# Performance work log

Hardware: AMD Instinct MI355X
Metric: run time of the kernel (lower is better)

The kernel has to match this reference:

```python
import jax, jax.numpy as jnp
import numpy as np

B, N, C = 4, 4096, 1024
H, M = 16, 64          # num_heads, num_landmarks
DH = C // H
SCALE = H ** (-0.5)    # faithful to source: num_heads**-0.5
LN_EPS = 1e-5


def setup_inputs() -> dict:
    key = jax.random.key(0)
    ks = jax.random.split(key, 8)
    s = 0.02
    return {
        "x": jax.random.normal(ks[0], (B, N, C), jnp.float32),
        "ln_w": jnp.ones((C,), jnp.float32),
        "ln_b": jnp.zeros((C,), jnp.float32),
        "qkv_w": jax.random.normal(ks[1], (3 * C, C), jnp.float32) * s,
        "qkv_b": jax.random.normal(ks[2], (3 * C,), jnp.float32) * s,
        "gamma_w": jax.random.normal(ks[3], (C, C), jnp.float32) * s,
        "gamma_b": jax.random.normal(ks[4], (C,), jnp.float32) * s,
        "proj_w": jax.random.normal(ks[5], (C, C), jnp.float32) * s,
        "proj_b": jax.random.normal(ks[6], (C,), jnp.float32) * s,
    }


def _iterative_inv(K, n_iter=6):
    # Newton-Schulz pseudo-inverse on [..., M, M]
    Id = jnp.eye(K.shape[-1], dtype=K.dtype)
    KA = jnp.abs(K)
    V0 = KA.sum(axis=-2, keepdims=True).max(axis=-1, keepdims=True)
    VI = KA.sum(axis=-1, keepdims=True).max(axis=-2, keepdims=True)
    V = jnp.swapaxes(K, -2, -1) / (V0 * VI)
    for _ in range(n_iter):
        KV = K @ V
        V = 0.25 * V @ (13.0 * Id - KV @ (15.0 * Id - KV @ (7.0 * Id - KV)))
    return V


def reference(x, ln_w, ln_b, qkv_w, qkv_b, gamma_w, gamma_b, proj_w, proj_b):
    # LayerNorm
    mu = x.mean(axis=-1, keepdims=True)
    var = x.var(axis=-1, keepdims=True)
    xn = (x - mu) * jax.lax.rsqrt(var + LN_EPS) * ln_w + ln_b
    # qkv: (B,N,3C) -> (3,B,H,N,DH)
    qkv = (xn @ qkv_w.T + qkv_b).reshape(B, N, 3, H, DH).transpose(2, 0, 3, 1, 4)
    q, k, v = qkv[0], qkv[1], qkv[2]
    # landmarks: mean-pool segments of length N//M, then scale
    q_lm = q.reshape(B, H, M, N // M, DH).mean(axis=-2) * SCALE  # (B,H,M,DH)
    k_lm = k.reshape(B, H, M, N // M, DH).mean(axis=-2) * SCALE
    attn1 = jax.nn.softmax(jnp.einsum('bhnd,bhmd->bhnm', q, k_lm), axis=-1)    # (B,H,N,M)
    attn2 = jax.nn.softmax(jnp.einsum('bhmd,bhld->bhml', q_lm, k_lm), axis=-1)  # (B,H,M,M)
    attn3 = jax.nn.softmax(jnp.einsum('bhmd,bhnd->bhmn', q_lm, k), axis=-1)    # (B,H,M,N)
    attn2_inv = _iterative_inv(attn2)
    out = attn1 @ (attn2_inv @ (attn3 @ v))            # (B,H,N,DH)
    out = out.transpose(0, 2, 1, 3).reshape(B, N, C)
    out = out @ gamma_w.T + gamma_b                    # LipNorm=True branch
    out = out @ proj_w.T + proj_b                      # proj (dropout p=0 is identity)
    return out
```

## Files before the change

### kernel.cpp

```cpp
#include <hip/hip_runtime.h>
#include <stdint.h>

typedef unsigned short u16;
typedef short bf16x8 __attribute__((ext_vector_type(8)));
typedef float f32x4 __attribute__((ext_vector_type(4)));

#define MFMA16(a, b, c) __builtin_amdgcn_mfma_f32_16x16x32_bf16((a), (b), (c), 0, 0, 0)

static __device__ __forceinline__ float bfu2f(u16 u) {
  union { unsigned int i; float f; } z; z.i = ((unsigned int)u) << 16; return z.f;
}
static __device__ __forceinline__ u16 f2bfu(float f) {
  union { float f; unsigned int i; } z; z.f = f;
  unsigned int i = z.i;
  return (u16)((i + 0x7fffu + ((i >> 16) & 1u)) >> 16);
}

__device__ __forceinline__ void gload_lds16(const void* g, void* l) {
  __builtin_amdgcn_global_load_lds((const __attribute__((address_space(1))) void*)g,
                                   (__attribute__((address_space(3))) void*)l, 16, 0, 0);
}

__global__ __launch_bounds__(256) void prep_kernel(
    const float* __restrict__ x, const float* __restrict__ lw,
    const float* __restrict__ lb, u16* __restrict__ xn,
    const float* __restrict__ qkvw, u16* __restrict__ QKVW,
    const float* __restrict__ projw, u16* __restrict__ PW,
    const float* __restrict__ G, u16* __restrict__ GT,
    const float* __restrict__ gb, const float* __restrict__ pb,
    float* __restrict__ b2) {
  int blk = blockIdx.x;
  int t = threadIdx.x;
  if (blk < 16384) {
    int row = blk;
    const float4* xr = (const float4*)(x + (size_t)row * 1024);
    float4 v = xr[t];
    float s = v.x + v.y + v.z + v.w;
    float ss = v.x * v.x + v.y * v.y + v.z * v.z + v.w * v.w;
#pragma unroll
    for (int m = 1; m < 64; m <<= 1) { s += __shfl_xor(s, m); ss += __shfl_xor(ss, m); }
    __shared__ float sb[4], ssb[4];
    int lane = t & 63, wvi = t >> 6;
    if (lane == 0) { sb[wvi] = s; ssb[wvi] = ss; }
    __syncthreads();
    s = sb[0] + sb[1] + sb[2] + sb[3];
    ss = ssb[0] + ssb[1] + ssb[2] + ssb[3];
    float mu = s * (1.0f / 1024.0f);
    float var = ss * (1.0f / 1024.0f) - mu * mu;
    float rstd = rsqrtf(var + 1e-5f);
    float4 wv4 = ((const float4*)lw)[t];
    float4 bv4 = ((const float4*)lb)[t];
    ushort4 o;
    o.x = f2bfu((v.x - mu) * rstd * wv4.x + bv4.x);
    o.y = f2bfu((v.y - mu) * rstd * wv4.y + bv4.y);
    o.z = f2bfu((v.z - mu) * rstd * wv4.z + bv4.z);
    o.w = f2bfu((v.w - mu) * rstd * wv4.w + bv4.w);
    ((ushort4*)xn)[(size_t)row * 256 + t] = o;
  } else if (blk < 18432) {
    int idx = (blk - 16384) * 256 + t;
    for (int i = idx; i < 1048576; i += 524288) {
      int j = i << 2;
      const float* s2; u16* d; int off;
      if (j < 3145728) { s2 = qkvw; d = QKVW; off = j; }
      else             { s2 = projw; d = PW; off = j - 3145728; }
      float4 v = *(const float4*)(s2 + off);
      ushort4 o;
      o.x = f2bfu(v.x); o.y = f2bfu(v.y); o.z = f2bfu(v.z); o.w = f2bfu(v.w);
      *(ushort4*)(d + off) = o;
    }
  } else if (blk < 18688) {
    __shared__ float tt[64][65];
    int tg = blk - 18432;
    int tr = (tg >> 4) * 64, tc = (tg & 15) * 64;
    int l = t & 63, y = t >> 6;
    for (int r = y; r < 64; r += 4)
      tt[r][l] = G[(size_t)(tr + r) * 1024 + tc + l];
    __syncthreads();
    for (int rr = y; rr < 64; rr += 4)
      GT[(size_t)(tc + rr) * 1024 + tr + l] = f2bfu(tt[l][rr]);
  } else {
    int i = (blk - 18688) * 256 + t;
    const float4* pr = (const float4*)(projw + (size_t)i * 1024);
    const float4* g4 = (const float4*)gb;
    float s = 0.f;
    for (int k = 0; k < 256; ++k) {
      float4 a = pr[k], b = g4[k];
      s += a.x * b.x + a.y * b.y + a.z * b.z + a.w * b.w;
    }
    b2[i] = s + pb[i];
  }
}

template <int MODE>
__global__ __launch_bounds__(512, 2) void gemm_bt(
    const u16* __restrict__ A, const u16* __restrict__ Bw,
    const float* __restrict__ bias,
    float* __restrict__ Cf, u16* __restrict__ Cb,
    u16* __restrict__ Qo, u16* __restrict__ Ko, u16* __restrict__ Vo,
    float* __restrict__ qlmf, u16* __restrict__ qlmb,
    float* __restrict__ klmf, u16* __restrict__ klmb,
    int M, int N, int K) {
  __shared__ __attribute__((aligned(16))) u16 As[2][16384];
  __shared__ __attribute__((aligned(16))) u16 Bs[2][16384];
  int tid = threadIdx.x;
  int lane = tid & 63;
  int w = tid >> 6;
  int wr = w >> 2, wc = w & 3;
  int r16 = lane & 15, hi = lane >> 4;
  int l8 = lane >> 3, li = lane & 7;

  int nwg = gridDim.x * gridDim.y;
  int flat = blockIdx.y * gridDim.x + blockIdx.x;
  int q8 = nwg >> 3;
  int swz = (flat & 7) * q8 + (flat >> 3);
  int bx = swz % gridDim.x, by = swz / gridDim.x;

  const char* Abase = (const char*)(A + (size_t)by * 256 * K);
  const char* Bbase = (const char*)(Bw + (size_t)bx * 256 * K);
  size_t rowbytes = (size_t)K * 2;
  int colsw = (li ^ l8) << 4;
  int nkt = K >> 6;

  f32x4 z4 = {0.f, 0.f, 0.f, 0.f};
  f32x4 acc[8][4];
#pragma unroll
  for (int m = 0; m < 8; ++m)
#pragma unroll
    for (int n = 0; n < 4; ++n) acc[m][n] = z4;

#define SG_A(buf, t, r0)                                                      \
  gload_lds16(Abase + (size_t)((r0) + w * 8 + l8) * rowbytes + ((t) << 7) +   \
                  colsw,                                                      \
              (char*)As[buf] + ((r0) + w * 8) * 128)
#define SG_B(buf, t, r0)                                                      \
  gload_lds16(Bbase + (size_t)((r0) + w * 8 + l8) * rowbytes + ((t) << 7) +   \
                  colsw,                                                      \
              (char*)Bs[buf] + ((r0) + w * 8) * 128)

  SG_A(0, 0, 0); SG_A(0, 0, 64); SG_A(0, 0, 128); SG_A(0, 0, 192);
  SG_B(0, 0, 0); SG_B(0, 0, 64); SG_B(0, 0, 128); SG_B(0, 0, 192);
  SG_A(1, 1, 0); SG_A(1, 1, 128); SG_B(1, 1, 0); SG_B(1, 1, 64);
  SG_A(1, 1, 64); SG_A(1, 1, 192);
  asm volatile("s_waitcnt vmcnt(6)" ::: "memory");
  __builtin_amdgcn_s_barrier();
  __builtin_amdgcn_sched_barrier(0);

  int buf = 0;
  bf16x8 af[4][2], bfr[4][2];

#define LDA(mh)                                                               \
  _Pragma("unroll") for (int m = 0; m < 4; ++m) {                             \
    int row = wr * 128 + (mh) * 64 + m * 16 + r16;                            \
    int sw = (row & 7) << 4;                                                  \
    _Pragma("unroll") for (int kk = 0; kk < 2; ++kk)                          \
        af[m][kk] = *(const bf16x8*)(ab + row * 128 +                         \
                                     (((kk << 6) | (hi << 4)) ^ sw));         \
  }
#define LDB(nh)                                                               \
  _Pragma("unroll") for (int n = 0; n < 2; ++n) {                             \
    int row = wc * 64 + (nh) * 32 + n * 16 + r16;                             \
    int sw = (row & 7) << 4;                                                  \
    _Pragma("unroll") for (int kk = 0; kk < 2; ++kk)                          \
        bfr[(nh) * 2 + n][kk] = *(const bf16x8*)(ab2 + row * 128 +            \
                                     (((kk << 6) | (hi << 4)) ^ sw));         \
  }
#define MM(mh, nh)                                                            \
  __builtin_amdgcn_s_setprio(1);                                              \
  _Pragma("unroll") for (int kk = 0; kk < 2; ++kk)                            \
      _Pragma("unroll") for (int m = 0; m < 4; ++m)                           \
          _Pragma("unroll") for (int n = 0; n < 2; ++n)                       \
              acc[(mh) * 4 + m][(nh) * 2 + n] =                               \
      MFMA16(af[m][kk], bfr[(nh) * 2 + n][kk], acc[(mh) * 4 + m][(nh) * 2 + n]); \
  __builtin_amdgcn_s_setprio(0)

#define BAR1                                                                  \
  __builtin_amdgcn_s_barrier();                                               \
  __builtin_amdgcn_sched_barrier(0)
#define BAR2                                                                  \
  __builtin_amdgcn_sched_barrier(0);                                          \
  __builtin_amdgcn_s_barrier();                                               \
  __builtin_amdgcn_sched_barrier(0)

  for (int t = 0; t < nkt; ++t) {
    const char* ab = (const char*)As[buf];
    const char* ab2 = (const char*)Bs[buf];
    bool s1 = (t + 1 < nkt), s2 = (t + 2 < nkt);
    LDA(0);
    LDB(0);
    if (s1) { SG_B(buf ^ 1, t + 1, 128); SG_B(buf ^ 1, t + 1, 192); }
    BAR1;
    MM(0, 0);
    BAR2;
    LDB(1);
    if (s2) { SG_A(buf, t + 2, 0); SG_A(buf, t + 2, 128); }
    BAR1;
    MM(0, 1);
    BAR2;
    LDA(1);
    if (s2) { SG_B(buf, t + 2, 0); SG_B(buf, t + 2, 64); }
    BAR1;
    MM(1, 0);
    BAR2;
    if (s2) { SG_A(buf, t + 2, 64); SG_A(buf, t + 2, 192); }
    BAR1;
    MM(1, 1);
    __builtin_amdgcn_sched_barrier(0);
    if (s2) {
      asm volatile("s_waitcnt vmcnt(6)" ::: "memory");
    } else {
      asm volatile("s_waitcnt vmcnt(0)" ::: "memory");
    }
    __builtin_amdgcn_s_barrier();
    __builtin_amdgcn_sched_barrier(0);
    buf ^= 1;
  }
#undef SG_A
#undef SG_B
#undef LDA
#undef LDB
#undef MM
#undef BAR1
#undef BAR2

#pragma unroll
  for (int m = 0; m < 8; ++m)
#pragma unroll
    for (int n = 0; n < 4; ++n) {
      int row0 = by * 256 + wr * 128 + m * 16 + hi * 4;
      int col = bx * 256 + wc * 64 + n * 16 + r16;
      if (MODE == 2) {
        int jt = col >> 10;
        int h = (col >> 6) & 15, dh = col & 63;
        int bb = row0 >> 12, nt0 = row0 & 4095;
        float bcol = bias[col];
        if (jt == 2) {
          ushort4 o;
          o.x = f2bfu(acc[m][n][0] + bcol);
          o.y = f2bfu(acc[m][n][1] + bcol);
          o.z = f2bfu(acc[m][n][2] + bcol);
          o.w = f2bfu(acc[m][n][3] + bcol);
          *(ushort4*)&Vo[(((size_t)bb * 16 + h) * 64 + dh) * 4096 + nt0] = o;
        } else {
          u16* dst = (jt == 0) ? Qo : Ko;
#pragma unroll
          for (int r = 0; r < 4; ++r)
            dst[(((size_t)bb * 16 + h) * 4096 + nt0 + r) * 64 + dh] =
                f2bfu(acc[m][n][r] + bcol);
        }
      } else {
        float bcol = bias[col];
#pragma unroll
        for (int r = 0; r < 4; ++r) {
          int row = row0 + r;
          Cf[(size_t)row * N + col] = acc[m][n][r] + bcol;
        }
      }
    }

  if (MODE == 2) {
    int jt = bx >> 2;
    if (jt < 2) {
      float* fo = (jt == 0) ? qlmf : klmf;
      u16* bo = (jt == 0) ? qlmb : klmb;
      int bb = by >> 4;
      int segb = (by * 4) & 63;
#pragma unroll
      for (int mh = 0; mh < 2; ++mh) {
        int seg = segb + wr * 2 + mh;
#pragma unroll
        for (int n = 0; n < 4; ++n) {
          int col = bx * 256 + wc * 64 + n * 16 + r16;
          float s = 0.f;
#pragma unroll
          for (int m = 0; m < 4; ++m)
#pragma unroll
            for (int r = 0; r < 4; ++r) s += acc[mh * 4 + m][n][r];
          s += 16.0f * bias[col];
          s += __shfl_xor(s, 16);
          s += __shfl_xor(s, 32);
          if (hi == 0) {
            int h = (col >> 6) & 15, dh = col & 63;
            float val = s * (0.25f / 64.0f);
            size_t o = (((size_t)bb * 16 + h) * 64 + seg) * 64 + dh;
            fo[o] = val;
            bo[o] = f2bfu(val);
          }
        }
      }
    }
  }
}

__global__ __launch_bounds__(256) void attn3_pv_kernel(
    const u16* __restrict__ qlmb, const u16* __restrict__ Kmat,
    const u16* __restrict__ Vt, float* __restrict__ Upart,
    float* __restrict__ rspart,
    const u16* __restrict__ Aw2, const u16* __restrict__ Bw2,
    float* __restrict__ Cp) {
  __shared__ __attribute__((aligned(16))) u16 Elds[4][8192];
  int tid = threadIdx.x, lane = tid & 63, w = tid >> 6;
  int r16 = lane & 15, hi = lane >> 4;
  int l8 = lane >> 3, li = lane & 7;

  if (blockIdx.x >= 4) {
    int wid = (blockIdx.x - 4) * 64 + blockIdx.y;
    u16* As = &Elds[0][0];
    u16* Bs = &Elds[1][0];
    int wr = w >> 1, wc = w & 1;
    int kz = wid >> 6, bxw = wid & 7, byw = (wid >> 3) & 7;
    const char* Abase = (const char*)(Aw2 + (size_t)byw * 131072 + kz * 256);
    const char* Bbase = (const char*)(Bw2 + (size_t)bxw * 131072 + kz * 256);
    int colsw = (li ^ l8) << 4;
    f32x4 z4 = {0.f, 0.f, 0.f, 0.f};
    f32x4 acc[4][4];
#pragma unroll
    for (int m = 0; m < 4; ++m)
#pragma unroll
      for (int n = 0; n < 4; ++n) acc[m][n] = z4;
    for (int kt = 0; kt < 4; ++kt) {
      int kb = kt << 7;
#pragma unroll
      for (int i = 0; i < 4; ++i) {
        int c = w * 4 + i;
        int rr = c * 8 + l8;
        gload_lds16(Abase + (size_t)rr * 2048 + kb + colsw, (char*)As + c * 1024);
        gload_lds16(Bbase + (size_t)rr * 2048 + kb + colsw, (char*)Bs + c * 1024);
      }
      __syncthreads();
      int sw = (lane & 7) << 4;
#pragma unroll
      for (int kk = 0; kk < 2; ++kk) {
        int kby = (kk << 6) + (hi << 4);
        bf16x8 af[4], bfr[4];
#pragma unroll
        for (int m = 0; m < 4; ++m) {
          int row = wr * 64 + m * 16 + r16;
          af[m] = *(const bf16x8*)((const char*)As + row * 128 + (kby ^ sw));
        }
#pragma unroll
        for (int n = 0; n < 4; ++n) {
          int row = wc * 64 + n * 16 + r16;
          bfr[n] = *(const bf16x8*)((const char*)Bs + row * 128 + (kby ^ sw));
        }
#pragma unroll
        for (int m = 0; m < 4; ++m)
#pragma unroll
          for (int n = 0; n < 4; ++n) acc[m][n] = MFMA16(af[m], bfr[n], acc[m][n]);
      }
      __syncthreads();
    }
#pragma unroll
    for (int m = 0; m < 4; ++m)
#pragma unroll
      for (int n = 0; n < 4; ++n)
#pragma unroll
        for (int r = 0; r < 4; ++r) {
          int row = byw * 128 + wr * 64 + m * 16 + hi * 4 + r;
          int col = bxw * 128 + wc * 64 + n * 16 + r16;
          Cp[(size_t)kz * 1048576 + (size_t)row * 1024 + col] = acc[m][n][r];
        }
    return;
  }

  int chunk = blockIdx.x, bh = blockIdx.y;
  const u16* vtb = Vt + (size_t)bh * 262144;
  const u16* qb = qlmb + (size_t)bh * 4096;
  u16* eb = &Elds[w][0];
  f32x4 z4 = {0.f, 0.f, 0.f, 0.f};

  bf16x8 afr[4][2];
#pragma unroll
  for (int m = 0; m < 4; ++m)
#pragma unroll
    for (int kk = 0; kk < 2; ++kk)
      afr[m][kk] = *(const bf16x8*)(qb + (m * 16 + r16) * 64 + kk * 32 + hi * 8);

  float rs[4][4] = {};
  f32x4 U[4][4];
#pragma unroll
  for (int m = 0; m < 4; ++m)
#pragma unroll
    for (int df = 0; df < 4; ++df) U[m][df] = z4;

  for (int bat = 0; bat < 2; ++bat) {
    int keybase = chunk * 1024 + bat * 512 + w * 128;
    const u16* kb = Kmat + ((size_t)bh * 4096 + keybase) * 64;
    for (int cf = 0; cf < 8; ++cf) {
      f32x4 S[4] = {z4, z4, z4, z4};
#pragma unroll
      for (int kk = 0; kk < 2; ++kk) {
        bf16x8 bfr = *(const bf16x8*)(kb + (size_t)(cf * 16 + r16) * 64 + kk * 32 + hi * 8);
#pragma unroll
        for (int m = 0; m < 4; ++m) S[m] = MFMA16(afr[m][kk], bfr, S[m]);
      }
#pragma unroll
      for (int m = 0; m < 4; ++m)
#pragma unroll
        for (int r = 0; r < 4; ++r) {
          float e = __expf(S[m][r]);
          rs[m][r] += e;
          int row = m * 16 + hi * 4 + r;
          int key = cf * 16 + r16;
          *(u16*)((char*)eb + row * 256 + ((key * 2) ^ ((row & 7) << 4))) = f2bfu(e);
        }
    }
    __syncthreads();
    for (int ks = 0; ks < 4; ++ks) {
      bf16x8 ea[4];
#pragma unroll
      for (int m = 0; m < 4; ++m) {
        int row = m * 16 + r16;
        ea[m] = *(const bf16x8*)((char*)eb + row * 256 + (((ks * 32 + hi * 8) * 2) ^ ((row & 7) << 4)));
      }
#pragma unroll
      for (int df = 0; df < 4; ++df) {
        bf16x8 vb8 = *(const bf16x8*)(vtb + (size_t)(df * 16 + r16) * 4096 +
                                      keybase + ks * 32 + hi * 8);
#pragma unroll
        for (int m = 0; m < 4; ++m) U[m][df] = MFMA16(ea[m], vb8, U[m][df]);
      }
    }
    __syncthreads();
  }

#pragma unroll
  for (int m = 0; m < 4; ++m)
#pragma unroll
    for (int r = 0; r < 4; ++r) {
      float v = rs[m][r];
      v += __shfl_xor(v, 1); v += __shfl_xor(v, 2);
      v += __shfl_xor(v, 4); v += __shfl_xor(v, 8);
      rs[m][r] = v;
    }
  if (r16 == 0) {
    float* rp = rspart + (((size_t)bh * 4 + chunk) * 4 + w) * 64;
#pragma unroll
    for (int m = 0; m < 4; ++m)
#pragma unroll
      for (int r = 0; r < 4; ++r) rp[m * 16 + hi * 4 + r] = rs[m][r];
  }
  float* up = Upart + (((size_t)bh * 4 + chunk) * 4 + w) * 4096;
#pragma unroll
  for (int m = 0; m < 4; ++m)
#pragma unroll
    for (int df = 0; df < 4; ++df)
#pragma unroll
      for (int r = 0; r < 4; ++r)
        up[(m * 16 + hi * 4 + r) * 64 + df * 16 + r16] = U[m][df][r];
}

__device__ __forceinline__ void mm64d(const float (*AT)[68], const float (*Bm)[68],
                                      float (*C)[68], float (*CT)[68],
                                      float alpha, float dconst, bool dmode,
                                      int tid) {
  int tr = (tid >> 4) << 1;
  int tc = (tid & 15) << 2;
  float acc[2][4] = {};
#pragma unroll 4
  for (int k = 0; k < 64; ++k) {
    float2 av = *(const float2*)&AT[k][tr];
    float4 bv = *(const float4*)&Bm[k][tc];
    float aa[2] = {av.x, av.y};
    float bb[4] = {bv.x, bv.y, bv.z, bv.w};
#pragma unroll
    for (int i = 0; i < 2; ++i)
#pragma unroll
      for (int j = 0; j < 4; ++j) acc[i][j] = fmaf(aa[i], bb[j], acc[i][j]);
  }
#pragma unroll
  for (int i = 0; i < 2; ++i)
#pragma unroll
    for (int j = 0; j < 4; ++j) {
      float vv = acc[i][j] * alpha;
      if (CT) CT[tc + j][tr + i] = vv;
      C[tr + i][tc + j] =
          dmode ? (((tr + i) == (tc + j)) ? dconst - vv : -vv) : vv;
    }
}

__global__ __launch_bounds__(512) void combine_ns_kernel(
    const float* __restrict__ Upart, const float* __restrict__ rspart,
    const float* __restrict__ qlmf, const float* __restrict__ klmf,
    u16* __restrict__ WT, const float* __restrict__ Cp,
    u16* __restrict__ W2b) {
  int tid = threadIdx.x;
  if (blockIdx.x >= 64) {
    int idx4 = (blockIdx.x - 64) * 512 + tid;
    const float4* p = (const float4*)Cp + idx4;
    float4 s = p[0];
    float4 b = p[262144], c = p[524288], d = p[786432];
    s.x += b.x + c.x + d.x;
    s.y += b.y + c.y + d.y;
    s.z += b.z + c.z + d.z;
    s.w += b.w + c.w + d.w;
    ushort4 o;
    o.x = f2bfu(s.x); o.y = f2bfu(s.y); o.z = f2bfu(s.z); o.w = f2bfu(s.w);
    ((ushort4*)W2b)[idx4] = o;
    return;
  }
  __shared__ __attribute__((aligned(16))) float A2T[64][68];
  __shared__ __attribute__((aligned(16))) float Vv[64][68];
  __shared__ __attribute__((aligned(16))) float VT[64][68];
  __shared__ __attribute__((aligned(16))) float KV[64][68];
  __shared__ __attribute__((aligned(16))) float KVT[64][68];
  __shared__ __attribute__((aligned(16))) float T2[64][68];
  __shared__ __attribute__((aligned(16))) float T4[64][68];
  __shared__ __attribute__((aligned(16))) float Tm[64][68];
  __shared__ float rsum[64], redbuf[64];
  __shared__ float scal;
  int bh = blockIdx.x;

  if (tid < 64) {
    float s = 0.f;
    const float* rp = rspart + (size_t)bh * 1024 + tid;
#pragma unroll 8
    for (int p = 0; p < 16; ++p) s += rp[p * 64];
    rsum[tid] = s;
  }
  __syncthreads();
  for (int idx4 = tid; idx4 < 1024; idx4 += 512) {
    const float4* up = (const float4*)(Upart + (size_t)bh * 65536) + idx4;
    float4 s = {0.f, 0.f, 0.f, 0.f};
#pragma unroll 8
    for (int p = 0; p < 16; ++p) {
      float4 v = up[p * 1024];
      s.x += v.x; s.y += v.y; s.z += v.z; s.w += v.w;
    }
    float inv = 1.0f / rsum[idx4 >> 4];
    int r = idx4 >> 4, c0 = (idx4 & 15) << 2;
    Tm[r][c0] = s.x * inv; Tm[r][c0 + 1] = s.y * inv;
    Tm[r][c0 + 2] = s.z * inv; Tm[r][c0 + 3] = s.w * inv;
  }
  for (int idx = tid; idx < 4096; idx += 512) {
    int r = idx >> 6, c = idx & 63;
    Vv[c][r] = qlmf[(size_t)bh * 4096 + idx];
    VT[c][r] = klmf[(size_t)bh * 4096 + idx];
  }
  __syncthreads();
  mm64d(&Vv[0], &VT[0], &T2[0], nullptr, 1.0f, 0.f, false, tid);
  __syncthreads();
  {
    int row = tid >> 3, sub = tid & 7, cb = sub * 8;
    float mx = -1e30f;
#pragma unroll
    for (int j = 0; j < 8; ++j) mx = fmaxf(mx, T2[row][cb + j]);
    mx = fmaxf(mx, __shfl_xor(mx, 1));
    mx = fmaxf(mx, __shfl_xor(mx, 2));
    mx = fmaxf(mx, __shfl_xor(mx, 4));
    float e[8];
    float s = 0.f;
#pragma unroll
    for (int j = 0; j < 8; ++j) { e[j] = __expf(T2[row][cb + j] - mx); s += e[j]; }
    s += __shfl_xor(s, 1); s += __shfl_xor(s, 2); s += __shfl_xor(s, 4);
    float inv = 1.f / s;
#pragma unroll
    for (int j = 0; j < 8; ++j) {
      float p = e[j] * inv;
      T2[row][cb + j] = p;
      A2T[cb + j][row] = p;
    }
  }
  __syncthreads();
  {
    int col = tid >> 3, sub = tid & 7;
    float cs = 0.f;
#pragma unroll
    for (int j = 0; j < 8; ++j) cs += T2[sub * 8 + j][col];
    cs += __shfl_xor(cs, 1); cs += __shfl_xor(cs, 2); cs += __shfl_xor(cs, 4);
    if (sub == 0) redbuf[col] = cs;
  }
  __syncthreads();
  if (tid < 64) {
    float v0 = redbuf[tid];
#pragma unroll
    for (int m = 1; m < 64; m <<= 1) v0 = fmaxf(v0, __shfl_xor(v0, m));
    if (tid == 0) scal = 1.0f / v0;
  }
  __syncthreads();
  for (int idx = tid; idx < 4096; idx += 512) {
    int r = idx >> 6, c = idx & 63;
    Vv[r][c] = A2T[r][c] * scal;
    VT[r][c] = T2[r][c] * scal;
  }
  __syncthreads();
  float (*Vt_r)[68] = VT;
  float (*Vt_w)[68] = KV;
#pragma unroll 1
  for (int it = 0; it < 6; ++it) {
    mm64d(&A2T[0], &Vv[0], &T2[0], &KVT[0], 1.0f, 7.0f, true, tid);
    __syncthreads();
    mm64d(&KVT[0], &T2[0], &T4[0], nullptr, 1.0f, 15.0f, true, tid);
    __syncthreads();
    mm64d(&KVT[0], &T4[0], &T2[0], nullptr, 1.0f, 13.0f, true, tid);
    __syncthreads();
    mm64d(Vt_r, &T2[0], &Vv[0], Vt_w, 0.25f, 0.f, false, tid);
    __syncthreads();
    float (*tmp)[68] = Vt_r; Vt_r = Vt_w; Vt_w = tmp;
  }
  mm64d(Vt_r, &Tm[0], &T2[0], nullptr, 1.0f, 0.f, false, tid);
  __syncthreads();
  for (int idx = tid; idx < 4096; idx += 512) {
    int r = idx >> 6, c = idx & 63;
    WT[(size_t)bh * 4096 + c * 64 + r] = f2bfu(T2[r][c]);
  }
}

__global__ __launch_bounds__(256) void attn1_out_kernel(
    const u16* __restrict__ Q, const u16* __restrict__ klmb,
    const u16* __restrict__ WT, u16* __restrict__ AO) {
  __shared__ __attribute__((aligned(16))) u16 Elds[4][2048];
  int bh = blockIdx.y;
  int b = bh >> 4, h = bh & 15;
  int tid = threadIdx.x, lane = tid & 63, w = tid >> 6;
  int r16 = lane & 15, hi = lane >> 4;
  int rowbase = blockIdx.x * 128 + w * 32;
  const u16* qb = Q + ((size_t)bh * 4096 + rowbase) * 64;
  const u16* kb = klmb + (size_t)bh * 4096;
  const u16* wtb = WT + (size_t)bh * 4096;
  u16* eb = &Elds[w][0];
  f32x4 z4 = {0.f, 0.f, 0.f, 0.f};

  bf16x8 afr[2][2];
#pragma unroll
  for (int mi = 0; mi < 2; ++mi)
#pragma unroll
    for (int kk = 0; kk < 2; ++kk)
      afr[mi][kk] = *(const bf16x8*)(qb + (mi * 16 + r16) * 64 + kk * 32 + hi * 8);

  float rs[2][4] = {};
  for (int cf = 0; cf < 4; ++cf) {
    f32x4 S[2] = {z4, z4};
#pragma unroll
    for (int kk = 0; kk < 2; ++kk) {
      bf16x8 bfr = *(const bf16x8*)(kb + (cf * 16 + r16) * 64 + kk * 32 + hi * 8);
#pragma unroll
      for (int mi = 0; mi < 2; ++mi) S[mi] = MFMA16(afr[mi][kk], bfr, S[mi]);
    }
#pragma unroll
    for (int mi = 0; mi < 2; ++mi)
#pragma unroll
      for (int r = 0; r < 4; ++r) {
        float e = __expf(S[mi][r]);
        rs[mi][r] += e;
        int row = mi * 16 + hi * 4 + r;
        int key = cf * 16 + r16;
        *(u16*)((char*)eb + row * 128 + ((key * 2) ^ ((row & 7) << 4))) = f2bfu(e);
      }
  }
#pragma unroll
  for (int mi = 0; mi < 2; ++mi)
#pragma unroll
    for (int r = 0; r < 4; ++r) {
      float v = rs[mi][r];
      v += __shfl_xor(v, 1); v += __shfl_xor(v, 2);
      v += __shfl_xor(v, 4); v += __shfl_xor(v, 8);
      rs[mi][r] = v;
    }
  __syncthreads();

  f32x4 O[2][4];
#pragma unroll
  for (int mi = 0; mi < 2; ++mi)
#pragma unroll
    for (int df = 0; df < 4; ++df) O[mi][df] = z4;
  for (int ks = 0; ks < 2; ++ks) {
    bf16x8 ea[2];
#pragma unroll
    for (int mi = 0; mi < 2; ++mi) {
      int row = mi * 16 + r16;
      ea[mi] = *(const bf16x8*)((char*)eb + row * 128 + (((ks * 32 + hi * 8) * 2) ^ ((row & 7) << 4)));
    }
#pragma unroll
    for (int df = 0; df < 4; ++df) {
      bf16x8 wfr = *(const bf16x8*)(wtb + (df * 16 + r16) * 64 + ks * 32 + hi * 8);
#pragma unroll
      for (int mi = 0; mi < 2; ++mi) O[mi][df] = MFMA16(ea[mi], wfr, O[mi][df]);
    }
  }
#pragma unroll
  for (int mi = 0; mi < 2; ++mi)
#pragma unroll
    for (int df = 0; df < 4; ++df)
#pragma unroll
      for (int r = 0; r < 4; ++r) {
        int row = mi * 16 + hi * 4 + r;
        int n = rowbase + row;
        int col = h * 64 + df * 16 + r16;
        float val = O[mi][df][r] / rs[mi][r];
        AO[((size_t)b * 4096 + n) * 1024 + col] = f2bfu(val);
      }
}

extern "C" void kernel_launch(void* const* d_in, const int* in_sizes, int n_in,
                              void* d_out, int out_size, void* d_ws, size_t ws_size,
                              hipStream_t stream) {
  (void)in_sizes; (void)n_in; (void)out_size; (void)ws_size;
  const float* x       = (const float*)d_in[0];
  const float* ln_w    = (const float*)d_in[1];
  const float* ln_b    = (const float*)d_in[2];
  const float* qkv_w   = (const float*)d_in[3];
  const float* qkv_b   = (const float*)d_in[4];
  const float* gamma_w = (const float*)d_in[5];
  const float* gamma_b = (const float*)d_in[6];
  const float* proj_w  = (const float*)d_in[7];
  const float* proj_b  = (const float*)d_in[8];

  char* ws = (char*)d_ws;
  u16* XN     = (u16*)(ws + 0);
  u16* Qb     = (u16*)(ws + 33554432);
  u16* Kb     = (u16*)(ws + 67108864);
  u16* Vb     = (u16*)(ws + 100663296);
  u16* QKVW   = (u16*)(ws + 134217728);
  u16* GTb    = (u16*)(ws + 140509184);
  u16* PW     = (u16*)(ws + 142606336);
  float* QLMF = (float*)(ws + 144703488);
  float* KLMF = (float*)(ws + 145752064);
  u16* QLMB   = (u16*)(ws + 146800640);
  u16* KLMB   = (u16*)(ws + 147324928);
  float* RSP  = (float*)(ws + 147849216);
  float* B2F  = (float*)(ws + 148111360);
  u16* WTb    = (u16*)(ws + 148373504);
  float* UP   = (float*)XN;
  float* CPF  = (float*)(ws + 16777216);
  u16* W2b    = (u16*)(ws + 102760448);

  prep_kernel<<<18692, 256, 0, stream>>>(x, ln_w, ln_b, XN, qkv_w, QKVW,
                                         proj_w, PW, gamma_w, GTb,
                                         gamma_b, proj_b, B2F);
  gemm_bt<2><<<dim3(12, 64), 512, 0, stream>>>(XN, QKVW, qkv_b, nullptr, nullptr,
                                               Qb, Kb, Vb, QLMF, QLMB, KLMF, KLMB,
                                               16384, 3072, 1024);
  attn3_pv_kernel<<<dim3(8, 64), 256, 0, stream>>>(QLMB, Kb, Vb, UP, RSP,
                                                   PW, GTb, CPF);
  combine_ns_kernel<<<576, 512, 0, stream>>>(UP, RSP, QLMF, KLMF, WTb, CPF, W2b);
  attn1_out_kernel<<<dim3(32, 64), 256, 0, stream>>>(Qb, KLMB, WTb, XN);
  gemm_bt<1><<<dim3(4, 64), 512, 0, stream>>>(XN, W2b, B2F, (float*)d_out, nullptr,
                                              nullptr, nullptr, nullptr,
                                              nullptr, nullptr, nullptr, nullptr,
                                              16384, 1024, 1024);
}
```

Measured before the change: 351.9 us.

## Move proj/gamma weight prep into QKV GEMM grid and halve attn3 key chunks

Moves the proj weight bf16 conversion, the gamma transpose and the fused bias computation out of the prep kernel into extra blocks (blockIdx.z==1) of the QKV GEMM launch, so this work overlaps the GEMM instead of lengthening prep. The attn3 kernel now processes 2048 keys per block over 2 chunks instead of 1024 over 4, which halves the partial U/rowsum buffers and the reduction work in the combine kernel. The trade-off is fewer attn3 blocks, so less parallelism and a longer serial loop per block.

```diff
diff --git a/kernel.cpp b/kernel.cpp
--- a/kernel.cpp
+++ b/kernel.cpp
@@ -24,11 +24,7 @@
 __global__ __launch_bounds__(256) void prep_kernel(
     const float* __restrict__ x, const float* __restrict__ lw,
     const float* __restrict__ lb, u16* __restrict__ xn,
-    const float* __restrict__ qkvw, u16* __restrict__ QKVW,
-    const float* __restrict__ projw, u16* __restrict__ PW,
-    const float* __restrict__ G, u16* __restrict__ GT,
-    const float* __restrict__ gb, const float* __restrict__ pb,
-    float* __restrict__ b2) {
+    const float* __restrict__ qkvw, u16* __restrict__ QKVW) {
   int blk = blockIdx.x;
   int t = threadIdx.x;
   if (blk < 16384) {
@@ -56,38 +52,14 @@
     o.z = f2bfu((v.z - mu) * rstd * wv4.z + bv4.z);
     o.w = f2bfu((v.w - mu) * rstd * wv4.w + bv4.w);
     ((ushort4*)xn)[(size_t)row * 256 + t] = o;
-  } else if (blk < 18432) {
+  } else {
     int idx = (blk - 16384) * 256 + t;
-    for (int i = idx; i < 1048576; i += 524288) {
-      int j = i << 2;
-      const float* s2; u16* d; int off;
-      if (j < 3145728) { s2 = qkvw; d = QKVW; off = j; }
-      else             { s2 = projw; d = PW; off = j - 3145728; }
-      float4 v = *(const float4*)(s2 + off);
+    for (int i = idx; i < 786432; i += 393216) {
+      float4 v = ((const float4*)qkvw)[i];
       ushort4 o;
       o.x = f2bfu(v.x); o.y = f2bfu(v.y); o.z = f2bfu(v.z); o.w = f2bfu(v.w);
-      *(ushort4*)(d + off) = o;
-    }
-  } else if (blk < 18688) {
-    __shared__ float tt[64][65];
-    int tg = blk - 18432;
-    int tr = (tg >> 4) * 64, tc = (tg & 15) * 64;
-    int l = t & 63, y = t >> 6;
-    for (int r = y; r < 64; r += 4)
-      tt[r][l] = G[(size_t)(tr + r) * 1024 + tc + l];
-    __syncthreads();
-    for (int rr = y; rr < 64; rr += 4)
-      GT[(size_t)(tc + rr) * 1024 + tr + l] = f2bfu(tt[l][rr]);
-  } else {
-    int i = (blk - 18688) * 256 + t;
-    const float4* pr = (const float4*)(projw + (size_t)i * 1024);
-    const float4* g4 = (const float4*)gb;
-    float s = 0.f;
-    for (int k = 0; k < 256; ++k) {
-      float4 a = pr[k], b = g4[k];
-      s += a.x * b.x + a.y * b.y + a.z * b.z + a.w * b.w;
-    }
-    b2[i] = s + pb[i];
+      ((ushort4*)QKVW)[i] = o;
+    }
   }
 }
 
@@ -99,6 +71,10 @@
     u16* __restrict__ Qo, u16* __restrict__ Ko, u16* __restrict__ Vo,
     float* __restrict__ qlmf, u16* __restrict__ qlmb,
     float* __restrict__ klmf, u16* __restrict__ klmb,
+    const float* __restrict__ projw, u16* __restrict__ PW,
+    const float* __restrict__ G, u16* __restrict__ GT,
+    const float* __restrict__ gb, const float* __restrict__ pb,
+    float* __restrict__ b2,
     int M, int N, int K) {
   __shared__ __attribute__((aligned(16))) u16 As[2][16384];
   __shared__ __attribute__((aligned(16))) u16 Bs[2][16384];
@@ -108,6 +84,40 @@
   int wr = w >> 2, wc = w & 3;
   int r16 = lane & 15, hi = lane >> 4;
   int l8 = lane >> 3, li = lane & 7;
+
+  if (MODE == 2 && blockIdx.z == 1) {
+    int e = blockIdx.y * 12 + blockIdx.x;
+    if (e < 512) {
+      int i = e * 512 + tid;
+      float4 v = ((const float4*)projw)[i];
+      ushort4 o;
+      o.x = f2bfu(v.x); o.y = f2bfu(v.y); o.z = f2bfu(v.z); o.w = f2bfu(v.w);
+      ((ushort4*)PW)[i] = o;
+    } else if (e < 640) {
+      float (*tt)[68] = (float (*)[68])As;
+      int half = tid >> 8;
+      int t2 = tid & 255;
+      int tile = (e - 512) * 2 + half;
+      int tr = (tile >> 4) * 64, tc = (tile & 15) * 64;
+      int l = t2 & 63, y = t2 >> 6;
+      for (int r = y; r < 64; r += 4)
+        tt[half * 64 + r][l] = G[(size_t)(tr + r) * 1024 + tc + l];
+      __syncthreads();
+      for (int rr = y; rr < 64; rr += 4)
+        GT[(size_t)(tc + rr) * 1024 + tr + l] = f2bfu(tt[half * 64 + l][rr]);
+    } else if (e < 642) {
+      int i = (e - 640) * 512 + tid;
+      const float4* pr = (const float4*)(projw + (size_t)i * 1024);
+      const float4* g4 = (const float4*)gb;
+      float s = 0.f;
+      for (int k = 0; k < 256; ++k) {
+        float4 a = pr[k], b = g4[k];
+        s += a.x * b.x + a.y * b.y + a.z * b.z + a.w * b.w;
+      }
+      b2[i] = s + pb[i];
+    }
+    return;
+  }
 
   int nwg = gridDim.x * gridDim.y;
   int flat = blockIdx.y * gridDim.x + blockIdx.x;
@@ -302,8 +312,8 @@
   int r16 = lane & 15, hi = lane >> 4;
   int l8 = lane >> 3, li = lane & 7;
 
-  if (blockIdx.x >= 4) {
-    int wid = (blockIdx.x - 4) * 64 + blockIdx.y;
+  if (blockIdx.x >= 2) {
+    int wid = (blockIdx.x - 2) * 64 + blockIdx.y;
     u16* As = &Elds[0][0];
     u16* Bs = &Elds[1][0];
     int wr = w >> 1, wc = w & 1;
@@ -382,8 +392,8 @@
 #pragma unroll
     for (int df = 0; df < 4; ++df) U[m][df] = z4;
 
-  for (int bat = 0; bat < 2; ++bat) {
-    int keybase = chunk * 1024 + bat * 512 + w * 128;
+  for (int bat = 0; bat < 4; ++bat) {
+    int keybase = chunk * 2048 + bat * 512 + w * 128;
     const u16* kb = Kmat + ((size_t)bh * 4096 + keybase) * 64;
     for (int cf = 0; cf < 8; ++cf) {
       f32x4 S[4] = {z4, z4, z4, z4};
@@ -433,13 +443,13 @@
       rs[m][r] = v;
     }
   if (r16 == 0) {
-    float* rp = rspart + (((size_t)bh * 4 + chunk) * 4 + w) * 64;
+    float* rp = rspart + (((size_t)bh * 2 + chunk) * 4 + w) * 64;
 #pragma unroll
     for (int m = 0; m < 4; ++m)
 #pragma unroll
       for (int r = 0; r < 4; ++r) rp[m * 16 + hi * 4 + r] = rs[m][r];
   }
-  float* up = Upart + (((size_t)bh * 4 + chunk) * 4 + w) * 4096;
+  float* up = Upart + (((size_t)bh * 2 + chunk) * 4 + w) * 4096;
 #pragma unroll
   for (int m = 0; m < 4; ++m)
 #pragma unroll
@@ -512,17 +522,17 @@
 
   if (tid < 64) {
     float s = 0.f;
-    const float* rp = rspart + (size_t)bh * 1024 + tid;
+    const float* rp = rspart + (size_t)bh * 512 + tid;
 #pragma unroll 8
-    for (int p = 0; p < 16; ++p) s += rp[p * 64];
+    for (int p = 0; p < 8; ++p) s += rp[p * 64];
     rsum[tid] = s;
   }
   __syncthreads();
   for (int idx4 = tid; idx4 < 1024; idx4 += 512) {
-    const float4* up = (const float4*)(Upart + (size_t)bh * 65536) + idx4;
+    const float4* up = (const float4*)(Upart + (size_t)bh * 32768) + idx4;
     float4 s = {0.f, 0.f, 0.f, 0.f};
 #pragma unroll 8
-    for (int p = 0; p < 16; ++p) {
+    for (int p = 0; p < 8; ++p) {
       float4 v = up[p * 1024];
       s.x += v.x; s.y += v.y; s.z += v.z; s.w += v.w;
     }
@@ -724,18 +734,19 @@
   float* CPF  = (float*)(ws + 16777216);
   u16* W2b    = (u16*)(ws + 102760448);
 
-  prep_kernel<<<18692, 256, 0, stream>>>(x, ln_w, ln_b, XN, qkv_w, QKVW,
-                                         proj_w, PW, gamma_w, GTb,
-                                         gamma_b, proj_b, B2F);
-  gemm_bt<2><<<dim3(12, 64), 512, 0, stream>>>(XN, QKVW, qkv_b, nullptr, nullptr,
-                                               Qb, Kb, Vb, QLMF, QLMB, KLMF, KLMB,
-                                               16384, 3072, 1024);
-  attn3_pv_kernel<<<dim3(8, 64), 256, 0, stream>>>(QLMB, Kb, Vb, UP, RSP,
+  prep_kernel<<<17920, 256, 0, stream>>>(x, ln_w, ln_b, XN, qkv_w, QKVW);
+  gemm_bt<2><<<dim3(12, 64, 2), 512, 0, stream>>>(
+      XN, QKVW, qkv_b, nullptr, nullptr, Qb, Kb, Vb,
+      QLMF, QLMB, KLMF, KLMB,
+      proj_w, PW, gamma_w, GTb, gamma_b, proj_b, B2F,
+      16384, 3072, 1024);
+  attn3_pv_kernel<<<dim3(6, 64), 256, 0, stream>>>(QLMB, Kb, Vb, UP, RSP,
                                                    PW, GTb, CPF);
   combine_ns_kernel<<<576, 512, 0, stream>>>(UP, RSP, QLMF, KLMF, WTb, CPF, W2b);
   attn1_out_kernel<<<dim3(32, 64), 256, 0, stream>>>(Qb, KLMB, WTb, XN);
-  gemm_bt<1><<<dim3(4, 64), 512, 0, stream>>>(XN, W2b, B2F, (float*)d_out, nullptr,
-                                              nullptr, nullptr, nullptr,
-                                              nullptr, nullptr, nullptr, nullptr,
-                                              16384, 1024, 1024);
-}
+  gemm_bt<1><<<dim3(4, 64), 512, 0, stream>>>(
+      XN, W2b, B2F, (float*)d_out, nullptr, nullptr, nullptr, nullptr,
+      nullptr, nullptr, nullptr, nullptr,
+      nullptr, nullptr, nullptr, nullptr, nullptr, nullptr, nullptr,
+      16384, 1024, 1024);
+}
```

Result: slower. 376.6 us (+7.0%).
